# Performance work log

Hardware: AMD Instinct MI355X
Metric: run time of the kernel (lower is better)

Reference implementation:

```python
import jax, jax.numpy as jnp
import numpy as np

DIMENSIONS = 1000
NUM_LEVELS = 10
SIZE = 28
BATCH = 256
NUM_CLASSES = 10


def setup_inputs() -> dict:
    key = jax.random.key(0)
    k1, k2, k3 = jax.random.split(key, 3)
    # pixel values in [0, 1]
    x = jax.random.uniform(k1, (BATCH, SIZE, SIZE), dtype=jnp.float32)
    # fixed bipolar position hypervectors (bundle of x/y Level HVs); use +-1 like MAP HVs
    position = jnp.where(jax.random.normal(k2, (SIZE * SIZE, DIMENSIONS)) > 0, 1.0, -1.0).astype(jnp.float32)
    # Level value embedding table
    value_table = jnp.where(jax.random.normal(k3, (NUM_LEVELS, DIMENSIONS)) > 0, 1.0, -1.0).astype(jnp.float32)
    # classifier weight, initialized to zero in the original module
    W = jnp.zeros((NUM_CLASSES, DIMENSIONS), dtype=jnp.float32)
    return {"x": x, "position": position, "value_table": value_table, "W": W}


def reference(x, position, value_table, W):
    B = x.shape[0]
    xf = x.reshape(B, -1)  # [B, P] flatten
    # torchhd Level value_to_index with low=0, high=1
    idx = jnp.clip(jnp.round(xf * (NUM_LEVELS - 1)), 0, NUM_LEVELS - 1).astype(jnp.int32)
    hv = value_table[idx]                         # gather: [B, P, D]
    bound = position[None, :, :] * hv             # bind:   [B, P, D]
    s = jnp.sum(bound, axis=1)                    # multiset sum over pixels: [B, D]
    enc = jnp.where(s > 0, 1.0, -1.0).astype(x.dtype)  # hard_quantize
    logit = enc @ W.T                             # [B, num_classes]
    return logit
```

## Files before the change

kernel.cpp:

```cpp
#include <hip/hip_runtime.h>
#include <stdint.h>

#define DIMS   1000
#define NLEV   10
#define NPIX   784
#define NBATCH 256
#define NCLS   10
#define WPD    32
#define QPIX   196
#define NGRP   16
#define NPLANE 6

__global__ void pack_bits(const float* __restrict__ position,
                          const float* __restrict__ value_table,
                          uint32_t* __restrict__ ws_bits) {
    int i = blockIdx.x * blockDim.x + threadIdx.x;
    const int n_pos = NPIX * WPD;
    const int n_tot = n_pos + NLEV * WPD;
    if (i >= n_tot) return;
    const float* src;
    int row, w;
    if (i < n_pos) { row = i >> 5; w = i & 31; src = position; }
    else           { int k = i - n_pos; row = k >> 5; w = k & 31; src = value_table; }

    uint32_t bits = 0;
    const float4* s4 = (const float4*)(src + row * DIMS + w * 32);
    #pragma unroll
    for (int c = 0; c < 8; ++c) {
        int d = w * 32 + c * 4;
        if (d < DIMS) {
            float4 v = s4[c];
            bits |= (v.x > 0.f ? 1u : 0u) << (c * 4 + 0);
            bits |= (v.y > 0.f ? 1u : 0u) << (c * 4 + 1);
            bits |= (v.z > 0.f ? 1u : 0u) << (c * 4 + 2);
            bits |= (v.w > 0.f ? 1u : 0u) << (c * 4 + 3);
        }
    }
    ws_bits[i] = bits;
}

__global__ __launch_bounds__(512) void hdc_main(const float* __restrict__ x,
                                                const float* __restrict__ W,
                                                const uint32_t* __restrict__ ws_bits,
                                                float* __restrict__ out) {
    __shared__ alignas(16) uint32_t s_pos[QPIX * WPD];
    __shared__ alignas(16) uint32_t s_vt[NLEV * WPD];
    __shared__ uint32_t s_idx[NPIX];
    __shared__ uint32_t s_cnt[WPD * NGRP * NPLANE];
    __shared__ float    s_red[8][NCLS];

    const int b = blockIdx.x;
    const int t = threadIdx.x;

    for (int p = t; p < NPIX; p += 512) {
        float v = x[b * NPIX + p] * 9.0f;
        int l = (int)rintf(v);
        l = l < 0 ? 0 : (l > 9 ? 9 : l);
        s_idx[p] = (uint32_t)l;
    }
    {
        const uint4* src = (const uint4*)(ws_bits + NPIX * WPD);
        uint4* dst = (uint4*)s_vt;
        if (t < 80) dst[t] = src[t];
    }

    const int w = t & 31;
    const int g = t >> 5;
    uint32_t c0 = 0, c1 = 0, c2 = 0, c3 = 0, c4 = 0, c5 = 0;

    #pragma unroll
    for (int q = 0; q < 4; ++q) {
        {
            const uint4* src = (const uint4*)(ws_bits + (size_t)q * QPIX * WPD);
            uint4* dst = (uint4*)s_pos;
            for (int i = t; i < 1568; i += 512) dst[i] = src[i];
        }
        __syncthreads();
        const int npix = (g < 12) ? 12 : 13;
        #pragma unroll 4
        for (int k = 0; k < npix; ++k) {
            int pl = (k < 12) ? (g + 16 * k) : (192 + (g - 12));
            uint32_t l = s_idx[q * QPIX + pl];
            uint32_t bits = ~(s_pos[pl * WPD + w] ^ s_vt[l * WPD + w]);
            uint32_t carry = bits, tmp;
            tmp = c0 & carry; c0 ^= carry; carry = tmp;
            tmp = c1 & carry; c1 ^= carry; carry = tmp;
            tmp = c2 & carry; c2 ^= carry; carry = tmp;
            tmp = c3 & carry; c3 ^= carry; carry = tmp;
            tmp = c4 & carry; c4 ^= carry; carry = tmp;
            c5 ^= carry;
        }
        __syncthreads();
    }

    {
        int base = (w * NGRP + g) * NPLANE;
        s_cnt[base + 0] = c0; s_cnt[base + 1] = c1; s_cnt[base + 2] = c2;
        s_cnt[base + 3] = c3; s_cnt[base + 4] = c4; s_cnt[base + 5] = c5;
    }
    __syncthreads();

    float partial[NCLS];
    #pragma unroll
    for (int c = 0; c < NCLS; ++c) partial[c] = 0.f;

    if (t < 500) {
        float enc[2];
        #pragma unroll
        for (int j = 0; j < 2; ++j) {
            int d = 2 * t + j;
            int w2 = d >> 5, bit = d & 31;
            int cnt = 0;
            #pragma unroll
            for (int g2 = 0; g2 < NGRP; ++g2) {
                int base = (w2 * NGRP + g2) * NPLANE;
                #pragma unroll
                for (int i = 0; i < NPLANE; ++i)
                    cnt += (int)((s_cnt[base + i] >> bit) & 1u) << i;
            }
            enc[j] = (cnt > 392) ? 1.0f : -1.0f;
        }
        #pragma unroll
        for (int c = 0; c < NCLS; ++c) {
            const float2* wv = (const float2*)(W + c * DIMS + 2 * t);
            float2 wl = *wv;
            partial[c] = enc[0] * wl.x + enc[1] * wl.y;
        }
    }

    #pragma unroll
    for (int c = 0; c < NCLS; ++c) {
        #pragma unroll
        for (int off = 32; off > 0; off >>= 1)
            partial[c] += __shfl_down(partial[c], off);
    }
    const int lane = t & 63, wid = t >> 6;
    if (lane == 0) {
        #pragma unroll
        for (int c = 0; c < NCLS; ++c) s_red[wid][c] = partial[c];
    }
    __syncthreads();
    if (t < NCLS) {
        float acc = 0.f;
        #pragma unroll
        for (int v = 0; v < 8; ++v) acc += s_red[v][t];
        out[b * NCLS + t] = acc;
    }
}

extern "C" void kernel_launch(void* const* d_in, const int* in_sizes, int n_in,
                              void* d_out, int out_size, void* d_ws, size_t ws_size,
                              hipStream_t stream) {
    const float* x        = (const float*)d_in[0];
    const float* position = (const float*)d_in[1];
    const float* vtab     = (const float*)d_in[2];
    const float* W        = (const float*)d_in[3];
    float* out            = (float*)d_out;
    uint32_t* ws_bits     = (uint32_t*)d_ws;

    const int n_words = NPIX * WPD + NLEV * WPD;
    pack_bits<<<(n_words + 255) / 256, 256, 0, stream>>>(position, vtab, ws_bits);
    hdc_main<<<NBATCH, 512, 0, stream>>>(x, W, ws_bits, out);
}
```

Before: 74.93 us.

## Pack bits via wave ballot, use CSA adder tree and bit-sliced popcount reduction

The packing kernel is replaced by one that has each wave read whole rows coalesced and build 64-bit masks with ballot, instead of each thread reading a strided 128-byte chunk. The main kernel no longer stages position bits in LDS. It reads them directly from global memory, eight pixels at a time, and compresses them with a carry-save full-adder tree. The per-dimension counts are then merged as bit-sliced adders across lane halves and a shared-memory tree, and the threshold is evaluated with bitwise logic, which replaces the per-bit count loop over 96 words. Risks: the bit order of the ballot packing must match the 32-bit word indexing, the hand-derived comparison logic must be correct, and the global reads of position bits depend on cache behaviour.

```diff
diff --git a/kernel.cpp b/kernel.cpp
--- a/kernel.cpp
+++ b/kernel.cpp
@@ -7,46 +7,44 @@
 #define NBATCH 256
 #define NCLS   10
 #define WPD    32
-#define QPIX   196
-#define NGRP   16
-#define NPLANE 6
-
-__global__ void pack_bits(const float* __restrict__ position,
-                          const float* __restrict__ value_table,
-                          uint32_t* __restrict__ ws_bits) {
-    int i = blockIdx.x * blockDim.x + threadIdx.x;
-    const int n_pos = NPIX * WPD;
-    const int n_tot = n_pos + NLEV * WPD;
-    if (i >= n_tot) return;
-    const float* src;
-    int row, w;
-    if (i < n_pos) { row = i >> 5; w = i & 31; src = position; }
-    else           { int k = i - n_pos; row = k >> 5; w = k & 31; src = value_table; }
-
-    uint32_t bits = 0;
-    const float4* s4 = (const float4*)(src + row * DIMS + w * 32);
-    #pragma unroll
-    for (int c = 0; c < 8; ++c) {
-        int d = w * 32 + c * 4;
-        if (d < DIMS) {
-            float4 v = s4[c];
-            bits |= (v.x > 0.f ? 1u : 0u) << (c * 4 + 0);
-            bits |= (v.y > 0.f ? 1u : 0u) << (c * 4 + 1);
-            bits |= (v.z > 0.f ? 1u : 0u) << (c * 4 + 2);
-            bits |= (v.w > 0.f ? 1u : 0u) << (c * 4 + 3);
-        }
-    }
-    ws_bits[i] = bits;
+
+__global__ __launch_bounds__(256) void pack_ballot(const float* __restrict__ position,
+                                                   const float* __restrict__ value_table,
+                                                   uint64_t* __restrict__ ws64) {
+    const int t    = threadIdx.x;
+    const int lane = t & 63;
+    const int wv   = (blockIdx.x * 256 + t) >> 6;
+    const int nw   = (gridDim.x * 256) >> 6;
+    for (int r = wv; r < NPIX + NLEV; r += nw) {
+        const float* src = (r < NPIX) ? (position + (size_t)r * DIMS)
+                                      : (value_table + (size_t)(r - NPIX) * DIMS);
+        #pragma unroll
+        for (int k = 0; k < 16; ++k) {
+            int d = k * 64 + lane;
+            float v = (d < DIMS) ? src[d] : 0.f;
+            uint64_t m = __ballot(v > 0.f);
+            if (lane == 0) ws64[(size_t)r * 16 + k] = m;
+        }
+    }
+}
+
+__device__ __forceinline__ void fa(uint32_t a, uint32_t b, uint32_t cin,
+                                   uint32_t& s, uint32_t& c) {
+    uint32_t t = a ^ b;
+    s = t ^ cin;
+    c = (a & b) | (t & cin);
 }
 
 __global__ __launch_bounds__(512) void hdc_main(const float* __restrict__ x,
                                                 const float* __restrict__ W,
                                                 const uint32_t* __restrict__ ws_bits,
                                                 float* __restrict__ out) {
-    __shared__ alignas(16) uint32_t s_pos[QPIX * WPD];
-    __shared__ alignas(16) uint32_t s_vt[NLEV * WPD];
     __shared__ uint32_t s_idx[NPIX];
-    __shared__ uint32_t s_cnt[WPD * NGRP * NPLANE];
+    __shared__ uint32_t s_vt[NLEV * WPD];
+    __shared__ uint32_t s_cnt1[32 * 8 * 7];
+    __shared__ uint32_t s_cnt2[32 * 4 * 8];
+    __shared__ uint32_t s_cnt3[32 * 2 * 9];
+    __shared__ uint32_t s_cnt4_enc[32];
     __shared__ float    s_red[8][NCLS];
 
     const int b = blockIdx.x;
@@ -56,88 +54,148 @@
         float v = x[b * NPIX + p] * 9.0f;
         int l = (int)rintf(v);
         l = l < 0 ? 0 : (l > 9 ? 9 : l);
-        s_idx[p] = (uint32_t)l;
-    }
-    {
-        const uint4* src = (const uint4*)(ws_bits + NPIX * WPD);
-        uint4* dst = (uint4*)s_vt;
-        if (t < 80) dst[t] = src[t];
-    }
+        s_idx[p] = (uint32_t)(l * WPD);
+    }
+    if (t < NLEV * WPD) s_vt[t] = ws_bits[NPIX * WPD + t];
+    __syncthreads();
 
     const int w = t & 31;
     const int g = t >> 5;
-    uint32_t c0 = 0, c1 = 0, c2 = 0, c3 = 0, c4 = 0, c5 = 0;
-
-    #pragma unroll
-    for (int q = 0; q < 4; ++q) {
-        {
-            const uint4* src = (const uint4*)(ws_bits + (size_t)q * QPIX * WPD);
-            uint4* dst = (uint4*)s_pos;
-            for (int i = t; i < 1568; i += 512) dst[i] = src[i];
-        }
-        __syncthreads();
-        const int npix = (g < 12) ? 12 : 13;
-        #pragma unroll 4
-        for (int k = 0; k < npix; ++k) {
-            int pl = (k < 12) ? (g + 16 * k) : (192 + (g - 12));
-            uint32_t l = s_idx[q * QPIX + pl];
-            uint32_t bits = ~(s_pos[pl * WPD + w] ^ s_vt[l * WPD + w]);
-            uint32_t carry = bits, tmp;
-            tmp = c0 & carry; c0 ^= carry; carry = tmp;
-            tmp = c1 & carry; c1 ^= carry; carry = tmp;
-            tmp = c2 & carry; c2 ^= carry; carry = tmp;
-            tmp = c3 & carry; c3 ^= carry; carry = tmp;
-            tmp = c4 & carry; c4 ^= carry; carry = tmp;
-            c5 ^= carry;
-        }
-        __syncthreads();
-    }
-
+
+    uint32_t p0 = 0, p1 = 0, p2 = 0, p3 = 0, p4 = 0, p5 = 0;
+
+    for (int c = 0; c < 6; ++c) {
+        uint32_t idxv[8], posv[8], xv[8];
+        #pragma unroll
+        for (int j = 0; j < 8; ++j)
+            idxv[j] = s_idx[g + 128 * c + 16 * j];
+        #pragma unroll
+        for (int j = 0; j < 8; ++j)
+            posv[j] = ws_bits[(g + 128 * c + 16 * j) * WPD + w];
+        #pragma unroll
+        for (int j = 0; j < 8; ++j)
+            xv[j] = posv[j] ^ s_vt[idxv[j] + w];
+        uint32_t sa, ca, sb, cb, sc, cc, sd, cd, se, ce, sf, cf, cg;
+        fa(xv[0], xv[1], xv[2], sa, ca);
+        fa(xv[3], xv[4], xv[5], sb, cb);
+        fa(xv[6], xv[7], p0,   sc, cc);
+        fa(sa, sb, sc, p0, cd);
+        fa(ca, cb, cc, se, ce);
+        fa(se, cd, p1, p1, cf);
+        fa(ce, cf, p2, p2, cg);
+        uint32_t tmp = p3 & cg; p3 ^= cg;
+        uint32_t tm2 = p4 & tmp; p4 ^= tmp;
+        p5 ^= tm2;
+    }
     {
-        int base = (w * NGRP + g) * NPLANE;
-        s_cnt[base + 0] = c0; s_cnt[base + 1] = c1; s_cnt[base + 2] = c2;
-        s_cnt[base + 3] = c3; s_cnt[base + 4] = c4; s_cnt[base + 5] = c5;
+        uint32_t xb = ws_bits[(g + 768) * WPD + w] ^ s_vt[s_idx[g + 768] + w];
+        uint32_t c = xb, tmp;
+        tmp = p0 & c; p0 ^= c; c = tmp;
+        tmp = p1 & c; p1 ^= c; c = tmp;
+        tmp = p2 & c; p2 ^= c; c = tmp;
+        tmp = p3 & c; p3 ^= c; c = tmp;
+        tmp = p4 & c; p4 ^= c; c = tmp;
+        p5 ^= c;
+    }
+
+    {
+        uint32_t q0 = __shfl_down(p0, 32), q1 = __shfl_down(p1, 32),
+                 q2 = __shfl_down(p2, 32), q3 = __shfl_down(p3, 32),
+                 q4 = __shfl_down(p4, 32), q5 = __shfl_down(p5, 32);
+        uint32_t r0, r1, r2, r3, r4, r5, r6, c, tt;
+        c  = p0 & q0; r0 = p0 ^ q0;
+        tt = p1 ^ q1; r1 = tt ^ c; c = (p1 & q1) | (tt & c);
+        tt = p2 ^ q2; r2 = tt ^ c; c = (p2 & q2) | (tt & c);
+        tt = p3 ^ q3; r3 = tt ^ c; c = (p3 & q3) | (tt & c);
+        tt = p4 ^ q4; r4 = tt ^ c; c = (p4 & q4) | (tt & c);
+        tt = p5 ^ q5; r5 = tt ^ c; c = (p5 & q5) | (tt & c);
+        r6 = c;
+        const int wid = t >> 6;
+        if ((t & 63) < 32) {
+            int base = (w * 8 + wid) * 7;
+            s_cnt1[base + 0] = r0; s_cnt1[base + 1] = r1; s_cnt1[base + 2] = r2;
+            s_cnt1[base + 3] = r3; s_cnt1[base + 4] = r4; s_cnt1[base + 5] = r5;
+            s_cnt1[base + 6] = r6;
+        }
+    }
+    __syncthreads();
+
+    if (t < 128) {
+        int w2 = t & 31, j = t >> 5;
+        int ba = (w2 * 8 + 2 * j) * 7, bb = (w2 * 8 + 2 * j + 1) * 7;
+        uint32_t c = 0, tt;
+        int bo = (w2 * 4 + j) * 8;
+        #pragma unroll
+        for (int i = 0; i < 7; ++i) {
+            uint32_t a = s_cnt1[ba + i], bv = s_cnt1[bb + i];
+            tt = a ^ bv; s_cnt2[bo + i] = tt ^ c; c = (a & bv) | (tt & c);
+        }
+        s_cnt2[bo + 7] = c;
+    }
+    __syncthreads();
+
+    if (t < 64) {
+        int w2 = t & 31, j = t >> 5;
+        int ba = (w2 * 4 + 2 * j) * 8, bb = (w2 * 4 + 2 * j + 1) * 8;
+        uint32_t c = 0, tt;
+        int bo = (w2 * 2 + j) * 9;
+        #pragma unroll
+        for (int i = 0; i < 8; ++i) {
+            uint32_t a = s_cnt2[ba + i], bv = s_cnt2[bb + i];
+            tt = a ^ bv; s_cnt3[bo + i] = tt ^ c; c = (a & bv) | (tt & c);
+        }
+        s_cnt3[bo + 8] = c;
+    }
+    __syncthreads();
+
+    if (t < 32) {
+        int ba = (t * 2) * 9, bb = (t * 2 + 1) * 9;
+        uint32_t cnt[10];
+        uint32_t c = 0, tt;
+        #pragma unroll
+        for (int i = 0; i < 9; ++i) {
+            uint32_t a = s_cnt3[ba + i], bv = s_cnt3[bb + i];
+            tt = a ^ bv; cnt[i] = tt ^ c; c = (a & bv) | (tt & c);
+        }
+        cnt[9] = c;
+        uint32_t cy = 0;
+        cy = cnt[3];
+        cy = cnt[4] | cy;
+        cy = cnt[5] | cy;
+        cy = cnt[6] | cy;
+        cy = cnt[7] & cy;
+        cy = cnt[8] & cy;
+        cy = cnt[9] | cy;
+        s_cnt4_enc[t] = ~cy;
     }
     __syncthreads();
 
     float partial[NCLS];
     #pragma unroll
-    for (int c = 0; c < NCLS; ++c) partial[c] = 0.f;
+    for (int cc = 0; cc < NCLS; ++cc) partial[cc] = 0.f;
 
     if (t < 500) {
-        float enc[2];
-        #pragma unroll
-        for (int j = 0; j < 2; ++j) {
-            int d = 2 * t + j;
-            int w2 = d >> 5, bit = d & 31;
-            int cnt = 0;
-            #pragma unroll
-            for (int g2 = 0; g2 < NGRP; ++g2) {
-                int base = (w2 * NGRP + g2) * NPLANE;
-                #pragma unroll
-                for (int i = 0; i < NPLANE; ++i)
-                    cnt += (int)((s_cnt[base + i] >> bit) & 1u) << i;
-            }
-            enc[j] = (cnt > 392) ? 1.0f : -1.0f;
-        }
-        #pragma unroll
-        for (int c = 0; c < NCLS; ++c) {
-            const float2* wv = (const float2*)(W + c * DIMS + 2 * t);
+        int d0 = 2 * t;
+        uint32_t ew = s_cnt4_enc[d0 >> 5];
+        float e0 = ((ew >> (d0 & 31)) & 1u) ? 1.0f : -1.0f;
+        float e1 = ((ew >> ((d0 + 1) & 31)) & 1u) ? 1.0f : -1.0f;
+        #pragma unroll
+        for (int cc = 0; cc < NCLS; ++cc) {
+            const float2* wv = (const float2*)(W + cc * DIMS + d0);
             float2 wl = *wv;
-            partial[c] = enc[0] * wl.x + enc[1] * wl.y;
-        }
-    }
-
+            partial[cc] = e0 * wl.x + e1 * wl.y;
+        }
+    }
     #pragma unroll
-    for (int c = 0; c < NCLS; ++c) {
+    for (int cc = 0; cc < NCLS; ++cc) {
         #pragma unroll
         for (int off = 32; off > 0; off >>= 1)
-            partial[c] += __shfl_down(partial[c], off);
+            partial[cc] += __shfl_down(partial[cc], off);
     }
     const int lane = t & 63, wid = t >> 6;
     if (lane == 0) {
         #pragma unroll
-        for (int c = 0; c < NCLS; ++c) s_red[wid][c] = partial[c];
+        for (int cc = 0; cc < NCLS; ++cc) s_red[wid][cc] = partial[cc];
     }
     __syncthreads();
     if (t < NCLS) {
@@ -156,9 +214,7 @@
     const float* vtab     = (const float*)d_in[2];
     const float* W        = (const float*)d_in[3];
     float* out            = (float*)d_out;
-    uint32_t* ws_bits     = (uint32_t*)d_ws;
-
-    const int n_words = NPIX * WPD + NLEV * WPD;
-    pack_bits<<<(n_words + 255) / 256, 256, 0, stream>>>(position, vtab, ws_bits);
-    hdc_main<<<NBATCH, 512, 0, stream>>>(x, W, ws_bits, out);
-}
+
+    pack_ballot<<<200, 256, 0, stream>>>(position, vtab, (uint64_t*)d_ws);
+    hdc_main<<<NBATCH, 512, 0, stream>>>(x, W, (const uint32_t*)d_ws, out);
+}
```

New measurement: 72.24 us. 3.6% less time.
